# Optimization experiments

Measured on AMD Instinct MI355X. Metric: run time of the kernel, lower is better.

Reference implementation:

```python
import jax, jax.numpy as jnp
import numpy as np


def _maxpool2x2(x):
    # x: [B, C, H, W] -> [B, C, H//2, W//2]
    B, C, H, W = x.shape
    return x.reshape(B, C, H // 2, 2, W // 2, 2).max(axis=(3, 5))


def setup_inputs() -> dict:
    key = jax.random.key(0)
    ks = jax.random.split(key, 6)
    B, C, H, W = 16, 64, 64, 64
    x = jax.random.normal(ks[0], (B, C, H, W), dtype=jnp.float32)
    w_theta = jax.random.normal(ks[1], (C // 8, C), dtype=jnp.float32) * (1.0 / np.sqrt(C))
    w_phi = jax.random.normal(ks[2], (C // 8, C), dtype=jnp.float32) * (1.0 / np.sqrt(C))
    w_g = jax.random.normal(ks[3], (C // 2, C), dtype=jnp.float32) * (1.0 / np.sqrt(C))
    w_o = jax.random.normal(ks[4], (C, C // 2), dtype=jnp.float32) * (1.0 / np.sqrt(C // 2))
    gamma = jax.random.normal(ks[5], (), dtype=jnp.float32)
    return {"x": x, "w_theta": w_theta, "w_phi": w_phi, "w_g": w_g, "w_o": w_o, "gamma": gamma}


def reference(x, w_theta, w_phi, w_g, w_o, gamma):
    B, C, H, W = x.shape
    S = H * W  # full spatial size
    # 1x1 convs == channel matmuls
    theta = jnp.einsum('oc,bchw->bohw', w_theta, x)            # [B, C/8, H, W]
    phi = _maxpool2x2(jnp.einsum('oc,bchw->bohw', w_phi, x))   # [B, C/8, H/2, W/2]
    g = _maxpool2x2(jnp.einsum('oc,bchw->bohw', w_g, x))       # [B, C/2, H/2, W/2]
    theta_f = theta.reshape(B, C // 8, S)                      # [B, C/8, S]
    phi_f = phi.reshape(B, C // 8, S // 4)                     # [B, C/8, S/4]
    g_f = g.reshape(B, C // 2, S // 4)                         # [B, C/2, S/4]
    # beta = softmax(theta^T @ phi) over key dim
    scores = jnp.einsum('bcs,bct->bst', theta_f, phi_f)        # [B, S, S/4]
    beta = jax.nn.softmax(scores, axis=-1)
    attn = jnp.einsum('bct,bst->bcs', g_f, beta)               # [B, C/2, S]
    o = jnp.einsum('oc,bcs->bos', w_o, attn).reshape(B, C, H, W)
    return gamma * o + x
```

## Files before the change

### kernel.cpp

```cpp
#include <hip/hip_runtime.h>

#define B 16
#define C 64
#define SS 4096
#define TT 1024
#define CQ 8
#define CG 32

typedef _Float16 h4 __attribute__((ext_vector_type(4)));
typedef float f32x16 __attribute__((ext_vector_type(16)));

#if __has_builtin(__builtin_amdgcn_exp2f)
#define EXP2(x) __builtin_amdgcn_exp2f(x)
#else
#define EXP2(x) exp2f(x)
#endif

#define MFMA328(a, b, c) __builtin_amdgcn_mfma_f32_32x32x8f16((a), (b), (c), 0, 0, 0)

__global__ __launch_bounds__(256) void k_proj(
        const float* __restrict__ x, const float* __restrict__ w_theta,
        const float* __restrict__ w_phi, const float* __restrict__ w_g,
        _Float16* __restrict__ theta_t, _Float16* __restrict__ phi_t,
        _Float16* __restrict__ g_blk) {
    int tid = threadIdx.x;
    int W = blockIdx.x * 4 + (tid >> 6);
    int l = tid & 63;
    int ln = l & 31, hi = l >> 5;
    int b = W >> 6, ws = W & 63;
    int rp = ws >> 1, wt = ws & 1;
    int sA = rp * 128 + wt * 32 + ln;

    const float LOG2E = 1.44269504088896f;
    float wsc = 1.f;
    const float* wr0;
    if (ln < 8)       { wr0 = w_theta + ln * C; wsc = LOG2E; }
    else if (ln < 16) { wr0 = w_phi + (ln - 8) * C; }
    else              { wr0 = w_g + (ln - 16) * C; }
    const float* wr1 = w_g + (16 + (ln & 15)) * C;
    bool t1v = ln < 16;

    h4 wa0[8], wa1[8];
#pragma unroll
    for (int kk = 0; kk < 8; ++kk) {
        float4 v0 = *(const float4*)&wr0[8 * kk + 4 * hi];
        float4 v1 = *(const float4*)&wr1[8 * kk + 4 * hi];
        wa0[kk][0] = (_Float16)(v0.x * wsc);
        wa0[kk][1] = (_Float16)(v0.y * wsc);
        wa0[kk][2] = (_Float16)(v0.z * wsc);
        wa0[kk][3] = (_Float16)(v0.w * wsc);
        wa1[kk][0] = t1v ? (_Float16)v1.x : (_Float16)0.f;
        wa1[kk][1] = t1v ? (_Float16)v1.y : (_Float16)0.f;
        wa1[kk][2] = t1v ? (_Float16)v1.z : (_Float16)0.f;
        wa1[kk][3] = t1v ? (_Float16)v1.w : (_Float16)0.f;
    }

    const float* xb = x + ((size_t)b << 18);
    float xA[8][4], xB[8][4];
#pragma unroll
    for (int kk = 0; kk < 8; ++kk)
#pragma unroll
        for (int i = 0; i < 4; ++i) {
            int c = 8 * kk + 4 * hi + i;
            xA[kk][i] = xb[((size_t)c << 12) + sA];
            xB[kk][i] = xb[((size_t)c << 12) + sA + 64];
        }

    f32x16 aA0, aA1, aB0, aB1;
#pragma unroll
    for (int r = 0; r < 16; ++r) { aA0[r] = 0.f; aA1[r] = 0.f; aB0[r] = 0.f; aB1[r] = 0.f; }

#pragma unroll
    for (int kk = 0; kk < 8; ++kk) {
        h4 bA, bB;
#pragma unroll
        for (int i = 0; i < 4; ++i) {
            bA[i] = (_Float16)xA[kk][i];
            bB[i] = (_Float16)xB[kk][i];
        }
        aA0 = MFMA328(wa0[kk], bA, aA0);
        aB0 = MFMA328(wa0[kk], bB, aB0);
        aA1 = MFMA328(wa1[kk], bA, aA1);
        aB1 = MFMA328(wa1[kk], bB, aB1);
    }

    {
        h4 tv;
#pragma unroll
        for (int r = 0; r < 4; ++r) tv[r] = (_Float16)aA0[r];
        *(h4*)&theta_t[(size_t)((b << 12) + sA) * 8 + 4 * hi] = tv;
#pragma unroll
        for (int r = 0; r < 4; ++r) tv[r] = (_Float16)aB0[r];
        *(h4*)&theta_t[(size_t)((b << 12) + sA + 64) * 8 + 4 * hi] = tv;
    }

    int t = rp * 32 + wt * 16 + (ln >> 1);
    float pv[4];
#pragma unroll
    for (int j = 0; j < 4; ++j) {
        float m = fmaxf(aA0[4 + j], aB0[4 + j]);
        m = fmaxf(m, __shfl_xor(m, 1));
        pv[j] = m;
    }
    float gv[4][4];
#pragma unroll
    for (int j = 0; j < 4; ++j) {
        float m0 = fmaxf(aA0[8 + j],  aB0[8 + j]);
        float m1 = fmaxf(aA0[12 + j], aB0[12 + j]);
        float m2 = fmaxf(aA1[j],      aB1[j]);
        float m3 = fmaxf(aA1[4 + j],  aB1[4 + j]);
        gv[0][j] = fmaxf(m0, __shfl_xor(m0, 1));
        gv[1][j] = fmaxf(m1, __shfl_xor(m1, 1));
        gv[2][j] = fmaxf(m2, __shfl_xor(m2, 1));
        gv[3][j] = fmaxf(m3, __shfl_xor(m3, 1));
    }
    if ((l & 1) == 0) {
        h4 pj;
#pragma unroll
        for (int j = 0; j < 4; ++j) pj[j] = (_Float16)pv[j];
        *(h4*)&phi_t[(size_t)((b << 10) + t) * 8 + 4 * hi] = pj;
        _Float16* gb = g_blk + ((size_t)(b * 256 + (t >> 2)) * 32) * 4 + (t & 3);
#pragma unroll
        for (int part = 0; part < 4; ++part) {
            int cbase = part * 8 + 4 * hi;
#pragma unroll
            for (int j = 0; j < 4; ++j)
                gb[(size_t)(cbase + j) * 4] = (_Float16)gv[part][j];
        }
    }
}

__global__ __launch_bounds__(512, 4) void k_attn(
        const float* __restrict__ x, const _Float16* __restrict__ theta_t,
        const _Float16* __restrict__ phi_t, const _Float16* __restrict__ g_blk,
        const float* __restrict__ w_o, const float* __restrict__ gamma_p,
        float* __restrict__ out) {
    __shared__ float accx[8][16][64];
    __shared__ float mlx[8][2][64];

    int tid = threadIdx.x;
    int bid = blockIdx.x;
    int wg = (bid & 7) * 64 + (bid >> 3);
    int b = wg >> 5;
    int s0 = (wg & 31) * 128;
    int w = tid >> 6;
    int l = tid & 63;
    int ln = l & 31, hi = l >> 5;
    int sub = w & 3, half = w >> 2;
    int sw = s0 + sub * 32;
    int h16 = half * 16;

    h4 bth = *(const h4*)&theta_t[(size_t)((b << 12) + sw + ln) * 8 + 4 * hi];

    const _Float16* phib = phi_t + ((size_t)b << 10) * 8;
    const _Float16* gbb  = g_blk + (size_t)b * (256 * 128);

    f32x16 zero;
#pragma unroll
    for (int r = 0; r < 16; ++r) zero[r] = 0.f;

#define LD_PHI(t_) (*(const h4*)&phib[(size_t)((t_) * 32 + ln) * 8 + 4 * hi])
#define LD_G(dst, t_)                                                          \
    {                                                                          \
        _Pragma("unroll")                                                      \
        for (int kk = 0; kk < 4; ++kk)                                         \
            dst[kk] = *(const h4*)&gbb[(size_t)(((t_) * 8 + 2 * kk + hi) * 32 + ln) * 4]; \
    }
#define FMAX16(dst, sc_)                                                       \
    {                                                                          \
        float y0 = fmaxf(sc_[0], sc_[1]),   y1 = fmaxf(sc_[2], sc_[3]);        \
        float y2 = fmaxf(sc_[4], sc_[5]),   y3 = fmaxf(sc_[6], sc_[7]);        \
        float y4 = fmaxf(sc_[8], sc_[9]),   y5 = fmaxf(sc_[10], sc_[11]);      \
        float y6 = fmaxf(sc_[12], sc_[13]), y7 = fmaxf(sc_[14], sc_[15]);      \
        y0 = fmaxf(y0, y1); y2 = fmaxf(y2, y3);                                \
        y4 = fmaxf(y4, y5); y6 = fmaxf(y6, y7);                                \
        y0 = fmaxf(y0, y2); y4 = fmaxf(y4, y6);                                \
        dst = fmaxf(dst, fmaxf(y0, y4));                                       \
    }

    float mx = -1e30f;
    {
        h4 pa = LD_PHI(h16);
        h4 pb = LD_PHI(h16 + 1);
#pragma unroll 2
        for (int tc = 0; tc < 16; tc += 2) {
            h4 pan = LD_PHI(h16 + ((tc + 2) & 15));
            h4 pbn = LD_PHI(h16 + ((tc + 3) & 15));
            f32x16 sa = MFMA328(pa, bth, zero);
            f32x16 sb = MFMA328(pb, bth, zero);
            FMAX16(mx, sa);
            FMAX16(mx, sb);
            pa = pan;
            pb = pbn;
        }
        mx = fmaxf(mx, __shfl_xor(mx, 32));
    }

    f32x16 cneg;
#pragma unroll
    for (int r = 0; r < 16; ++r) cneg[r] = -mx;

    f32x16 acc = zero;
    float lsum = 0.f;
    h4 ap = LD_PHI(h16);
    h4 ap2 = LD_PHI(h16 + 1);
    h4 ag[4], ag2[4];
    LD_G(ag, h16);
    LD_G(ag2, h16 + 1);

#pragma unroll 2
    for (int tc = 0; tc < 16; ++tc) {
        int tn = h16 + ((tc + 2) & 15);
        h4 apn = LD_PHI(tn);
        h4 agn[4];
        LD_G(agn, tn);

        f32x16 sc = MFMA328(ap, bth, cneg);

        h4 bp[4];
        float pa0 = 0.f, pa1 = 0.f;
#pragma unroll
        for (int kk = 0; kk < 4; ++kk)
#pragma unroll
            for (int i = 0; i < 4; ++i) {
                float p = EXP2(sc[4 * kk + i]);
                if (kk < 2) pa0 += p; else pa1 += p;
                bp[kk][i] = (_Float16)p;
            }
        lsum += pa0 + pa1;

#pragma unroll
        for (int kk = 0; kk < 4; ++kk) acc = MFMA328(ag[kk], bp[kk], acc);

        ap = ap2; ap2 = apn;
#pragma unroll
        for (int kk = 0; kk < 4; ++kk) { ag[kk] = ag2[kk]; ag2[kk] = agn[kk]; }
    }
    lsum += __shfl_xor(lsum, 32);

#pragma unroll
    for (int r = 0; r < 16; ++r) accx[w][r][l] = acc[r];
    mlx[w][0][l] = mx;
    mlx[w][1][l] = lsum;
    __syncthreads();

    int p = w ^ 4;
    float m2 = mlx[p][0][l], l2 = mlx[p][1][l];
    float M = fmaxf(mx, m2);
    float f1 = EXP2(mx - M), f2 = EXP2(m2 - M);
    float lt = lsum * f1 + l2 * f2;
    float linv = 1.f / lt;

    h4 bat[4];
#pragma unroll
    for (int kk = 0; kk < 4; ++kk)
#pragma unroll
        for (int i = 0; i < 4; ++i) {
            float a2 = accx[p][4 * kk + i][l];
            bat[kk][i] = (_Float16)((acc[4 * kk + i] * f1 + a2 * f2) * linv);
        }

    float gm = gamma_p[0];
    h4 a3[4];
#pragma unroll
    for (int kk = 0; kk < 4; ++kk) {
        float4 wv = *(const float4*)&w_o[(half * 32 + ln) * CG + 8 * kk + 4 * hi];
        a3[kk][0] = (_Float16)(wv.x * gm);
        a3[kk][1] = (_Float16)(wv.y * gm);
        a3[kk][2] = (_Float16)(wv.z * gm);
        a3[kk][3] = (_Float16)(wv.w * gm);
    }
    f32x16 d = MFMA328(a3[0], bat[0], zero);
    d = MFMA328(a3[1], bat[1], d);
    d = MFMA328(a3[2], bat[2], d);
    d = MFMA328(a3[3], bat[3], d);
#pragma unroll
    for (int r = 0; r < 16; ++r) {
        int ch = half * 32 + (r & 3) + 8 * (r >> 2) + 4 * hi;
        size_t idx = (((size_t)(b * C + ch)) << 12) + sw + ln;
        out[idx] = d[r] + x[idx];
    }
#undef LD_PHI
#undef LD_G
#undef FMAX16
}

extern "C" void kernel_launch(void* const* d_in, const int* in_sizes, int n_in,
                              void* d_out, int out_size, void* d_ws, size_t ws_size,
                              hipStream_t stream) {
    const float* x       = (const float*)d_in[0];
    const float* w_theta = (const float*)d_in[1];
    const float* w_phi   = (const float*)d_in[2];
    const float* w_g     = (const float*)d_in[3];
    const float* w_o     = (const float*)d_in[4];
    const float* gamma   = (const float*)d_in[5];
    float* out = (float*)d_out;

    _Float16* ws      = (_Float16*)d_ws;
    _Float16* theta_t = ws;
    _Float16* phi_t   = theta_t + (size_t)B * SS * 8;
    _Float16* g_blk   = phi_t + (size_t)B * TT * 8;

    k_proj<<<256, 256, 0, stream>>>(x, w_theta, w_phi, w_g, theta_t, phi_t, g_blk);
    k_attn<<<512, 512, 0, stream>>>(x, theta_t, phi_t, g_blk, w_o, gamma, out);
}
```

Baseline: 32.91 us.

## Halve attention block size and interleave two independent accumulator chains per wave

Each attention block now covers 64 query positions with 4 waves instead of 128 with 8, and the grid doubles to 1024 blocks. The inner softmax-PV loop processes two key chunks per iteration into separate accumulators, giving independent MFMA chains and exp work for latency hiding, then sums them at the end. Register use rises from the duplicated accumulators and prefetch buffers, and the launch bounds change to a 256-thread, 3-block minimum, which may lower occupancy.

```diff
diff --git a/kernel.cpp b/kernel.cpp
--- a/kernel.cpp
+++ b/kernel.cpp
@@ -130,23 +130,23 @@
     }
 }
 
-__global__ __launch_bounds__(512, 4) void k_attn(
+__global__ __launch_bounds__(256, 3) void k_attn(
         const float* __restrict__ x, const _Float16* __restrict__ theta_t,
         const _Float16* __restrict__ phi_t, const _Float16* __restrict__ g_blk,
         const float* __restrict__ w_o, const float* __restrict__ gamma_p,
         float* __restrict__ out) {
-    __shared__ float accx[8][16][64];
-    __shared__ float mlx[8][2][64];
+    __shared__ float accx[4][16][64];
+    __shared__ float mlx[4][2][64];
 
     int tid = threadIdx.x;
     int bid = blockIdx.x;
-    int wg = (bid & 7) * 64 + (bid >> 3);
-    int b = wg >> 5;
-    int s0 = (wg & 31) * 128;
+    int wg = (bid & 7) * 128 + (bid >> 3);
+    int b = wg >> 6;
+    int s0 = (wg & 63) * 64;
     int w = tid >> 6;
     int l = tid & 63;
     int ln = l & 31, hi = l >> 5;
-    int sub = w & 3, half = w >> 2;
+    int sub = w & 1, half = w >> 1;
     int sw = s0 + sub * 32;
     int h16 = half * 16;
 
@@ -200,42 +200,56 @@
 #pragma unroll
     for (int r = 0; r < 16; ++r) cneg[r] = -mx;
 
-    f32x16 acc = zero;
-    float lsum = 0.f;
-    h4 ap = LD_PHI(h16);
-    h4 ap2 = LD_PHI(h16 + 1);
-    h4 ag[4], ag2[4];
-    LD_G(ag, h16);
-    LD_G(ag2, h16 + 1);
+    f32x16 accA = zero, accB = zero;
+    float lsumA = 0.f, lsumB = 0.f;
+
+    h4 apA = LD_PHI(h16);
+    h4 apB = LD_PHI(h16 + 1);
+    h4 agA[4], agB[4];
+    LD_G(agA, h16);
+    LD_G(agB, h16 + 1);
 
 #pragma unroll 2
-    for (int tc = 0; tc < 16; ++tc) {
-        int tn = h16 + ((tc + 2) & 15);
-        h4 apn = LD_PHI(tn);
-        h4 agn[4];
-        LD_G(agn, tn);
-
-        f32x16 sc = MFMA328(ap, bth, cneg);
-
-        h4 bp[4];
-        float pa0 = 0.f, pa1 = 0.f;
+    for (int tc = 0; tc < 16; tc += 2) {
+        int t2 = h16 + ((tc + 2) & 15), t3 = h16 + ((tc + 3) & 15);
+        h4 apAn = LD_PHI(t2);
+        h4 apBn = LD_PHI(t3);
+        h4 agAn[4], agBn[4];
+        LD_G(agAn, t2);
+        LD_G(agBn, t3);
+
+        f32x16 scA = MFMA328(apA, bth, cneg);
+        f32x16 scB = MFMA328(apB, bth, cneg);
+
+        h4 bpA[4], bpB[4];
+        float pa0 = 0.f, pa1 = 0.f, pb0 = 0.f, pb1 = 0.f;
 #pragma unroll
         for (int kk = 0; kk < 4; ++kk)
 #pragma unroll
             for (int i = 0; i < 4; ++i) {
-                float p = EXP2(sc[4 * kk + i]);
-                if (kk < 2) pa0 += p; else pa1 += p;
-                bp[kk][i] = (_Float16)p;
+                float pA = EXP2(scA[4 * kk + i]);
+                float pB = EXP2(scB[4 * kk + i]);
+                if (kk < 2) { pa0 += pA; pb0 += pB; }
+                else        { pa1 += pA; pb1 += pB; }
+                bpA[kk][i] = (_Float16)pA;
+                bpB[kk][i] = (_Float16)pB;
             }
-        lsum += pa0 + pa1;
-
-#pragma unroll
-        for (int kk = 0; kk < 4; ++kk) acc = MFMA328(ag[kk], bp[kk], acc);
-
-        ap = ap2; ap2 = apn;
-#pragma unroll
-        for (int kk = 0; kk < 4; ++kk) { ag[kk] = ag2[kk]; ag2[kk] = agn[kk]; }
-    }
+        lsumA += pa0 + pa1;
+        lsumB += pb0 + pb1;
+
+#pragma unroll
+        for (int kk = 0; kk < 4; ++kk) accA = MFMA328(agA[kk], bpA[kk], accA);
+#pragma unroll
+        for (int kk = 0; kk < 4; ++kk) accB = MFMA328(agB[kk], bpB[kk], accB);
+
+        apA = apAn;
+        apB = apBn;
+#pragma unroll
+        for (int kk = 0; kk < 4; ++kk) { agA[kk] = agAn[kk]; agB[kk] = agBn[kk]; }
+    }
+
+    f32x16 acc = accA + accB;
+    float lsum = lsumA + lsumB;
     lsum += __shfl_xor(lsum, 32);
 
 #pragma unroll
@@ -244,7 +258,7 @@
     mlx[w][1][l] = lsum;
     __syncthreads();
 
-    int p = w ^ 4;
+    int p = w ^ 2;
     float m2 = mlx[p][0][l], l2 = mlx[p][1][l];
     float M = fmaxf(mx, m2);
     float f1 = EXP2(mx - M), f2 = EXP2(m2 - M);
@@ -302,5 +316,5 @@
     _Float16* g_blk   = phi_t + (size_t)B * TT * 8;
 
     k_proj<<<256, 256, 0, stream>>>(x, w_theta, w_phi, w_g, theta_t, phi_t, g_blk);
-    k_attn<<<512, 512, 0, stream>>>(x, theta_t, phi_t, g_blk, w_o, gamma, out);
+    k_attn<<<1024, 256, 0, stream>>>(x, theta_t, phi_t, g_blk, w_o, gamma, out);
 }
```

After: 35.04 us. 6.5% more time.

## Replace two-pass softmax max with online rescaling in attention loop

Applied to the files above, without the earlier changes.

Drops the separate pass that recomputed all score tiles just to find the row maximum, and switches to an online softmax that tracks a running max per tile and rescales the accumulator and sum when it grows. This saves one MFMA per tile plus the max-reduction pass. The cost is a per-tile max reduction, a cross-lane shuffle and a wave-uniform branch for rescaling inside the main loop, which adds to the loop's critical path.

```diff
diff --git a/kernel.cpp b/kernel.cpp
--- a/kernel.cpp
+++ b/kernel.cpp
@@ -178,44 +178,65 @@
         dst = fmaxf(dst, fmaxf(y0, y4));                                       \
     }
 
-    float mx = -1e30f;
-    {
-        h4 pa = LD_PHI(h16);
-        h4 pb = LD_PHI(h16 + 1);
-#pragma unroll 2
-        for (int tc = 0; tc < 16; tc += 2) {
-            h4 pan = LD_PHI(h16 + ((tc + 2) & 15));
-            h4 pbn = LD_PHI(h16 + ((tc + 3) & 15));
-            f32x16 sa = MFMA328(pa, bth, zero);
-            f32x16 sb = MFMA328(pb, bth, zero);
-            FMAX16(mx, sa);
-            FMAX16(mx, sb);
-            pa = pan;
-            pb = pbn;
-        }
-        mx = fmaxf(mx, __shfl_xor(mx, 32));
-    }
-
-    f32x16 cneg;
-#pragma unroll
-    for (int r = 0; r < 16; ++r) cneg[r] = -mx;
-
     f32x16 acc = zero;
     float lsum = 0.f;
+    float mx;
     h4 ap = LD_PHI(h16);
     h4 ap2 = LD_PHI(h16 + 1);
     h4 ag[4], ag2[4];
     LD_G(ag, h16);
     LD_G(ag2, h16 + 1);
 
+    {
+        h4 apn = LD_PHI(h16 + 2);
+        h4 agn[4];
+        LD_G(agn, h16 + 2);
+
+        f32x16 sc = MFMA328(ap, bth, zero);
+        float cm = -1e30f;
+        FMAX16(cm, sc);
+        cm = fmaxf(cm, __shfl_xor(cm, 32));
+        mx = cm;
+
+        h4 bp[4];
+        float pa0 = 0.f, pa1 = 0.f;
+#pragma unroll
+        for (int kk = 0; kk < 4; ++kk)
+#pragma unroll
+            for (int i = 0; i < 4; ++i) {
+                float p = EXP2(sc[4 * kk + i] - mx);
+                if (kk < 2) pa0 += p; else pa1 += p;
+                bp[kk][i] = (_Float16)p;
+            }
+        lsum = pa0 + pa1;
+#pragma unroll
+        for (int kk = 0; kk < 4; ++kk) acc = MFMA328(ag[kk], bp[kk], acc);
+
+        ap = ap2; ap2 = apn;
+#pragma unroll
+        for (int kk = 0; kk < 4; ++kk) { ag[kk] = ag2[kk]; ag2[kk] = agn[kk]; }
+    }
+
 #pragma unroll 2
-    for (int tc = 0; tc < 16; ++tc) {
+    for (int tc = 1; tc < 16; ++tc) {
         int tn = h16 + ((tc + 2) & 15);
         h4 apn = LD_PHI(tn);
         h4 agn[4];
         LD_G(agn, tn);
 
-        f32x16 sc = MFMA328(ap, bth, cneg);
+        f32x16 sc = MFMA328(ap, bth, zero);
+
+        float cm = -1e30f;
+        FMAX16(cm, sc);
+        cm = fmaxf(cm, __shfl_xor(cm, 32));
+        float nm = fmaxf(mx, cm);
+        if (__any(nm > mx)) {
+            float scl = EXP2(mx - nm);
+            mx = nm;
+            lsum *= scl;
+#pragma unroll
+            for (int r = 0; r < 16; ++r) acc[r] *= scl;
+        }
 
         h4 bp[4];
         float pa0 = 0.f, pa1 = 0.f;
@@ -223,7 +244,7 @@
         for (int kk = 0; kk < 4; ++kk)
 #pragma unroll
             for (int i = 0; i < 4; ++i) {
-                float p = EXP2(sc[4 * kk + i]);
+                float p = EXP2(sc[4 * kk + i] - mx);
                 if (kk < 2) pa0 += p; else pa1 += p;
                 bp[kk][i] = (_Float16)p;
             }
```

After: 33.66 us. +2.3%, slower.
